# Kernel optimization log

Hardware: AMD Instinct MI355X
Metric: run time of the kernel (lower is better)

Reference implementation:

```python
import jax, jax.numpy as jnp
import numpy as np

N = 100000      # nodes
E = 3200000     # directed edges (avg degree 32)
F_IN = 128      # node feature dim
H = 16          # hidden_features
A = 10          # num_actions


def setup_inputs() -> dict:
    key = jax.random.key(0)
    ks = jax.random.split(key, 8)
    x = jax.random.normal(ks[0], (N, F_IN), dtype=jnp.float32)
    edge_index = jax.random.randint(ks[1], (2, E), 0, N, dtype=jnp.int32)
    W1 = jax.random.normal(ks[2], (F_IN, H), dtype=jnp.float32) * (1.0 / np.sqrt(F_IN))
    b1 = jnp.zeros((H,), dtype=jnp.float32)
    W2 = jax.random.normal(ks[3], (H, H), dtype=jnp.float32) * (1.0 / np.sqrt(H))
    b2 = jnp.zeros((H,), dtype=jnp.float32)
    Wc = jax.random.normal(ks[4], (H, A), dtype=jnp.float32) * (1.0 / np.sqrt(H))
    bc = jnp.zeros((A,), dtype=jnp.float32)
    return {"x": x, "edge_index": edge_index, "W1": W1, "b1": b1,
            "W2": W2, "b2": b2, "Wc": Wc, "bc": bc}


def _gcn_norm(edge_index, n_nodes):
    # PyG GCNConv: add self-loops, symmetric normalization deg^-1/2 A_hat deg^-1/2
    loop = jnp.arange(n_nodes, dtype=edge_index.dtype)
    src = jnp.concatenate([edge_index[0], loop])   # message sources
    dst = jnp.concatenate([edge_index[1], loop])   # aggregation targets
    deg = jax.ops.segment_sum(jnp.ones_like(dst, dtype=jnp.float32), dst,
                              num_segments=n_nodes)
    dis = jnp.where(deg > 0, jax.lax.rsqrt(deg), 0.0)  # deg^-1/2, inf -> 0
    norm = dis[src] * dis[dst]                          # [E + N]
    return src, dst, norm


def _gcn_conv(h, W, b, src, dst, norm, n_nodes):
    # transform first (small output dim), then gather/scale/scatter-add
    msg = (h @ W)[src] * norm[:, None]                  # [E+N, out]
    return jax.ops.segment_sum(msg, dst, num_segments=n_nodes) + b


def reference(x, edge_index, W1, b1, W2, b2, Wc, bc):
    n_nodes = x.shape[0]
    src, dst, norm = _gcn_norm(edge_index, n_nodes)
    h = jax.nn.relu(_gcn_conv(x, W1, b1, src, dst, norm, n_nodes))
    # F.dropout(training=False) is identity at inference
    h = jax.nn.relu(_gcn_conv(h, W2, b2, src, dst, norm, n_nodes))
    pooled = jnp.max(h, axis=0)                         # global MaxAggregation -> [H]
    return pooled @ Wc + bc                             # squeeze() -> [A]
```

## Files before the change

kernel.cpp:

```cpp
#include <hip/hip_runtime.h>
#include <hip/hip_fp16.h>


#define FIN 128
#define HDIM 16
#define AOUT 10
#define NPB 256
#define KMAX 512
#define TILE 4096
#define CAP 9216

typedef _Float16 f16x8 __attribute__((ext_vector_type(8)));
typedef float f32x4 __attribute__((ext_vector_type(4)));

__global__ void k_init(int* __restrict__ bcur, unsigned int* __restrict__ pooled,
                       int K) {
    int i = blockIdx.x * 256 + threadIdx.x;
    if (i < K) bcur[i] = i * CAP;
    if (i < 16) pooled[i] = 0u;
}

__global__ __launch_bounds__(256) void k_bin(const int* __restrict__ src,
                                             const int* __restrict__ dst, int E,
                                             int* __restrict__ bcur,
                                             unsigned int* __restrict__ pairs, int K) {
    __shared__ int hist[KMAX], lofs[KMAX], run[KMAX], gbase[KMAX], ss[256];
    __shared__ unsigned int buf[TILE];
    __shared__ unsigned short bkt[TILE];
    int t = threadIdx.x;
    int e0 = blockIdx.x * TILE;
    int e1 = min(E, e0 + TILE);
    for (int i = t; i < KMAX; i += 256) hist[i] = 0;
    __syncthreads();
    for (int e = e0 + t * 4; e < e1; e += 1024) {
        if (e + 4 <= e1) {
            int4 d4 = *reinterpret_cast<const int4*>(dst + e);
            atomicAdd(&hist[d4.x >> 8], 1);
            atomicAdd(&hist[d4.y >> 8], 1);
            atomicAdd(&hist[d4.z >> 8], 1);
            atomicAdd(&hist[d4.w >> 8], 1);
        } else {
            for (int q = e; q < e1; q++) atomicAdd(&hist[dst[q] >> 8], 1);
        }
    }
    __syncthreads();
    int a0 = hist[2 * t], a1 = hist[2 * t + 1];
    int psum = a0 + a1;
    ss[t] = psum;
    for (int d = 1; d < 256; d <<= 1) {
        __syncthreads();
        int add = (t >= d) ? ss[t - d] : 0;
        __syncthreads();
        ss[t] += add;
    }
    __syncthreads();
    int excl = ss[t] - psum;
    lofs[2 * t] = excl;          run[2 * t] = excl;
    lofs[2 * t + 1] = excl + a0; run[2 * t + 1] = excl + a0;
    __syncthreads();
    for (int b = t; b < K; b += 256)
        if (hist[b]) gbase[b] = atomicAdd(&bcur[b], hist[b]);
    __syncthreads();
    for (int e = e0 + t * 4; e < e1; e += 1024) {
        if (e + 4 <= e1) {
            int4 d4 = *reinterpret_cast<const int4*>(dst + e);
            int4 s4 = *reinterpret_cast<const int4*>(src + e);
            int b, r;
            b = d4.x >> 8; r = atomicAdd(&run[b], 1);
            buf[r] = (unsigned)s4.x | ((unsigned)(d4.x & 255) << 17); bkt[r] = (unsigned short)b;
            b = d4.y >> 8; r = atomicAdd(&run[b], 1);
            buf[r] = (unsigned)s4.y | ((unsigned)(d4.y & 255) << 17); bkt[r] = (unsigned short)b;
            b = d4.z >> 8; r = atomicAdd(&run[b], 1);
            buf[r] = (unsigned)s4.z | ((unsigned)(d4.z & 255) << 17); bkt[r] = (unsigned short)b;
            b = d4.w >> 8; r = atomicAdd(&run[b], 1);
            buf[r] = (unsigned)s4.w | ((unsigned)(d4.w & 255) << 17); bkt[r] = (unsigned short)b;
        } else {
            for (int q = e; q < e1; q++) {
                int d = dst[q], s = src[q], b = d >> 8;
                int r = atomicAdd(&run[b], 1);
                buf[r] = (unsigned)s | ((unsigned)(d & 255) << 17);
                bkt[r] = (unsigned short)b;
            }
        }
    }
    __syncthreads();
    int m = e1 - e0;
    for (int i = t; i < m; i += 256) {
        int b = bkt[i];
        pairs[gbase[b] + i - lofs[b]] = buf[i];
    }
}

__global__ __launch_bounds__(512) void k_sort(const unsigned int* __restrict__ pairs,
                                              const int* __restrict__ bcur,
                                              int* __restrict__ srcidx,
                                              int2* __restrict__ off2,
                                              float* __restrict__ dis, int n) {
    __shared__ int lcnt[NPB], pre[NPB], cur[NPB];
    int b = blockIdx.x, t = threadIdx.x;
    if (t < NPB) lcnt[t] = 0;
    __syncthreads();
    int base = b * CAP;
    int m = bcur[b] - base;
    for (int j = t; j < m; j += 512) atomicAdd(&lcnt[pairs[base + j] >> 17], 1);
    __syncthreads();
    int v = (t < NPB) ? lcnt[t] : 0;
    if (t < NPB) pre[t] = v;
    for (int d = 1; d < NPB; d <<= 1) {
        __syncthreads();
        int add = (t < NPB && t >= d) ? pre[t - d] : 0;
        __syncthreads();
        if (t < NPB) pre[t] += add;
    }
    __syncthreads();
    if (t < NPB) {
        int excl = pre[t] - v;
        cur[t] = excl;
        int node = (b << 8) + t;
        if (node < n) {
            off2[node] = make_int2(base + excl, base + excl + v);
            dis[node] = rsqrtf((float)(v + 1));
        }
    }
    __syncthreads();
    for (int j = t; j < m; j += 512) {
        unsigned p = pairs[base + j];
        int pos = base + atomicAdd(&cur[p >> 17], 1);
        srcidx[pos] = (int)(p & 0x1FFFF);
    }
}

__global__ __launch_bounds__(256) void k_gemm1(const float* __restrict__ x,
                                               const float* __restrict__ W1,
                                               const float* __restrict__ dis,
                                               __half* __restrict__ g16, int n) {
    int l = threadIdx.x & 63;
    int cc = l & 15, kg = l >> 4;
    f16x8 bfrag[4];
#pragma unroll
    for (int kc = 0; kc < 4; kc++)
#pragma unroll
        for (int j = 0; j < 8; j++)
            bfrag[kc][j] = (_Float16)W1[(kc * 32 + kg * 8 + j) * HDIM + cc];
    int tile = blockIdx.x * 4 + (threadIdx.x >> 6);
    int node0 = tile * 16;
    if (node0 >= n) return;
    const float* xr = x + (size_t)(node0 + cc) * FIN;
    f32x4 acc = {0.f, 0.f, 0.f, 0.f};
#pragma unroll
    for (int kc = 0; kc < 4; kc++) {
        float4 xa = *reinterpret_cast<const float4*>(xr + kc * 32 + kg * 8);
        float4 xb = *reinterpret_cast<const float4*>(xr + kc * 32 + kg * 8 + 4);
        f16x8 a;
        a[0] = (_Float16)xa.x; a[1] = (_Float16)xa.y;
        a[2] = (_Float16)xa.z; a[3] = (_Float16)xa.w;
        a[4] = (_Float16)xb.x; a[5] = (_Float16)xb.y;
        a[6] = (_Float16)xb.z; a[7] = (_Float16)xb.w;
        acc = __builtin_amdgcn_mfma_f32_16x16x32_f16(a, bfrag[kc], acc, 0, 0, 0);
    }
#pragma unroll
    for (int i = 0; i < 4; i++) {
        int nd = node0 + kg * 4 + i;
        g16[(size_t)nd * HDIM + cc] = (__half)(dis[nd] * acc[i]);
    }
}

__global__ __launch_bounds__(256) void k_gemm2(const float* __restrict__ h,
                                               const float* __restrict__ W2,
                                               const float* __restrict__ dis,
                                               __half* __restrict__ g16, int n) {
    int l = threadIdx.x & 63;
    int cc = l & 15, kg = l >> 4;
    f16x8 bfrag = {0, 0, 0, 0, 0, 0, 0, 0};
    if (kg < 2) {
#pragma unroll
        for (int j = 0; j < 8; j++)
            bfrag[j] = (_Float16)W2[(kg * 8 + j) * HDIM + cc];
    }
    int tile = blockIdx.x * 4 + (threadIdx.x >> 6);
    int node0 = tile * 16;
    if (node0 >= n) return;
    f16x8 a = {0, 0, 0, 0, 0, 0, 0, 0};
    if (kg < 2) {
        const float* hr = h + (size_t)(node0 + cc) * HDIM + kg * 8;
        float4 xa = *reinterpret_cast<const float4*>(hr);
        float4 xb = *reinterpret_cast<const float4*>(hr + 4);
        a[0] = (_Float16)xa.x; a[1] = (_Float16)xa.y;
        a[2] = (_Float16)xa.z; a[3] = (_Float16)xa.w;
        a[4] = (_Float16)xb.x; a[5] = (_Float16)xb.y;
        a[6] = (_Float16)xb.z; a[7] = (_Float16)xb.w;
    }
    f32x4 acc = {0.f, 0.f, 0.f, 0.f};
    acc = __builtin_amdgcn_mfma_f32_16x16x32_f16(a, bfrag, acc, 0, 0, 0);
#pragma unroll
    for (int i = 0; i < 4; i++) {
        int nd = node0 + kg * 4 + i;
        g16[(size_t)nd * HDIM + cc] = (__half)(dis[nd] * acc[i]);
    }
}

__global__ __launch_bounds__(256) void k_agg16(const __half* __restrict__ g16,
                                               const int2* __restrict__ off2,
                                               const int* __restrict__ srcidx,
                                               const float* __restrict__ dis,
                                               const float* __restrict__ bias,
                                               float* __restrict__ h, int n) {
    int tid = blockIdx.x * 256 + threadIdx.x;
    int node = tid >> 2, sub = tid & 3;
    int piece = sub & 1, half = sub >> 1;
    if (node >= n) return;
    const uint4* gp = reinterpret_cast<const uint4*>(g16);
    int2 oe = off2[node];
    int e0 = oe.x, e1 = oe.y;
    __half2 a0, a1, a2, a3;
    if (half == 0) {
        uint4 v = gp[(size_t)node * 2 + piece];
        a0 = __builtin_bit_cast(__half2, v.x);
        a1 = __builtin_bit_cast(__half2, v.y);
        a2 = __builtin_bit_cast(__half2, v.z);
        a3 = __builtin_bit_cast(__half2, v.w);
    } else {
        a0 = __half2{0, 0}; a1 = __half2{0, 0};
        a2 = __half2{0, 0}; a3 = __half2{0, 0};
    }
    int e = e0 + half;
    for (; e + 14 < e1; e += 16) {
        int s0 = srcidx[e];      int s1 = srcidx[e + 2];
        int s2 = srcidx[e + 4];  int s3 = srcidx[e + 6];
        int s4 = srcidx[e + 8];  int s5 = srcidx[e + 10];
        int s6 = srcidx[e + 12]; int s7 = srcidx[e + 14];
        uint4 w0 = gp[(size_t)s0 * 2 + piece];
        uint4 w1 = gp[(size_t)s1 * 2 + piece];
        uint4 w2 = gp[(size_t)s2 * 2 + piece];
        uint4 w3 = gp[(size_t)s3 * 2 + piece];
        uint4 w4 = gp[(size_t)s4 * 2 + piece];
        uint4 w5 = gp[(size_t)s5 * 2 + piece];
        uint4 w6 = gp[(size_t)s6 * 2 + piece];
        uint4 w7 = gp[(size_t)s7 * 2 + piece];
        a0 = __hadd2(a0, __builtin_bit_cast(__half2, w0.x));
        a1 = __hadd2(a1, __builtin_bit_cast(__half2, w0.y));
        a2 = __hadd2(a2, __builtin_bit_cast(__half2, w0.z));
        a3 = __hadd2(a3, __builtin_bit_cast(__half2, w0.w));
        a0 = __hadd2(a0, __builtin_bit_cast(__half2, w1.x));
        a1 = __hadd2(a1, __builtin_bit_cast(__half2, w1.y));
        a2 = __hadd2(a2, __builtin_bit_cast(__half2, w1.z));
        a3 = __hadd2(a3, __builtin_bit_cast(__half2, w1.w));
        a0 = __hadd2(a0, __builtin_bit_cast(__half2, w2.x));
        a1 = __hadd2(a1, __builtin_bit_cast(__half2, w2.y));
        a2 = __hadd2(a2, __builtin_bit_cast(__half2, w2.z));
        a3 = __hadd2(a3, __builtin_bit_cast(__half2, w2.w));
        a0 = __hadd2(a0, __builtin_bit_cast(__half2, w3.x));
        a1 = __hadd2(a1, __builtin_bit_cast(__half2, w3.y));
        a2 = __hadd2(a2, __builtin_bit_cast(__half2, w3.z));
        a3 = __hadd2(a3, __builtin_bit_cast(__half2, w3.w));
        a0 = __hadd2(a0, __builtin_bit_cast(__half2, w4.x));
        a1 = __hadd2(a1, __builtin_bit_cast(__half2, w4.y));
        a2 = __hadd2(a2, __builtin_bit_cast(__half2, w4.z));
        a3 = __hadd2(a3, __builtin_bit_cast(__half2, w4.w));
        a0 = __hadd2(a0, __builtin_bit_cast(__half2, w5.x));
        a1 = __hadd2(a1, __builtin_bit_cast(__half2, w5.y));
        a2 = __hadd2(a2, __builtin_bit_cast(__half2, w5.z));
        a3 = __hadd2(a3, __builtin_bit_cast(__half2, w5.w));
        a0 = __hadd2(a0, __builtin_bit_cast(__half2, w6.x));
        a1 = __hadd2(a1, __builtin_bit_cast(__half2, w6.y));
        a2 = __hadd2(a2, __builtin_bit_cast(__half2, w6.z));
        a3 = __hadd2(a3, __builtin_bit_cast(__half2, w6.w));
        a0 = __hadd2(a0, __builtin_bit_cast(__half2, w7.x));
        a1 = __hadd2(a1, __builtin_bit_cast(__half2, w7.y));
        a2 = __hadd2(a2, __builtin_bit_cast(__half2, w7.z));
        a3 = __hadd2(a3, __builtin_bit_cast(__half2, w7.w));
    }
    for (; e < e1; e += 2) {
        uint4 w = gp[(size_t)srcidx[e] * 2 + piece];
        a0 = __hadd2(a0, __builtin_bit_cast(__half2, w.x));
        a1 = __hadd2(a1, __builtin_bit_cast(__half2, w.y));
        a2 = __hadd2(a2, __builtin_bit_cast(__half2, w.z));
        a3 = __hadd2(a3, __builtin_bit_cast(__half2, w.w));
    }
    a0 = __hadd2(a0, __builtin_bit_cast(__half2, __shfl_xor(__builtin_bit_cast(unsigned, a0), 2)));
    a1 = __hadd2(a1, __builtin_bit_cast(__half2, __shfl_xor(__builtin_bit_cast(unsigned, a1), 2)));
    a2 = __hadd2(a2, __builtin_bit_cast(__half2, __shfl_xor(__builtin_bit_cast(unsigned, a2), 2)));
    a3 = __hadd2(a3, __builtin_bit_cast(__half2, __shfl_xor(__builtin_bit_cast(unsigned, a3), 2)));
    if (half == 0) {
        float dn = dis[node];
        const float* bp = bias + piece * 8;
        float2 f0 = __half22float2(a0), f1 = __half22float2(a1);
        float2 f2 = __half22float2(a2), f3 = __half22float2(a3);
        float4 o0, o1;
        o0.x = fmaxf(dn * f0.x + bp[0], 0.f); o0.y = fmaxf(dn * f0.y + bp[1], 0.f);
        o0.z = fmaxf(dn * f1.x + bp[2], 0.f); o0.w = fmaxf(dn * f1.y + bp[3], 0.f);
        o1.x = fmaxf(dn * f2.x + bp[4], 0.f); o1.y = fmaxf(dn * f2.y + bp[5], 0.f);
        o1.z = fmaxf(dn * f3.x + bp[6], 0.f); o1.w = fmaxf(dn * f3.y + bp[7], 0.f);
        float4* hp = reinterpret_cast<float4*>(h + (size_t)node * HDIM + piece * 8);
        hp[0] = o0; hp[1] = o1;
    }
}

__global__ __launch_bounds__(256) void k_maxpool(const float* __restrict__ h,
                                                 unsigned int* __restrict__ pooled, int n) {
    int t = threadIdx.x;
    int c = t & 15;
    int grp = t >> 4;
    float m = 0.f;
    for (int node = blockIdx.x * 16 + grp; node < n; node += gridDim.x * 16)
        m = fmaxf(m, h[(size_t)node * HDIM + c]);
    __shared__ float s[256];
    s[t] = m;
    __syncthreads();
    for (int d = 128; d >= 16; d >>= 1) {
        if (t < d) s[t] = fmaxf(s[t], s[t + d]);
        __syncthreads();
    }
    if (t < 16) atomicMax(&pooled[t], __float_as_uint(s[t]));
}

__global__ void k_final(const unsigned int* __restrict__ pooled, const float* __restrict__ Wc,
                        const float* __restrict__ bc, float* __restrict__ out) {
    __shared__ float p[HDIM];
    int t = threadIdx.x;
    if (t < HDIM) p[t] = __uint_as_float(pooled[t]);
    __syncthreads();
    if (t < AOUT) {
        float acc = bc[t];
#pragma unroll
        for (int c = 0; c < HDIM; c++) acc += p[c] * Wc[c * AOUT + t];
        out[t] = acc;
    }
}

extern "C" void kernel_launch(void* const* d_in, const int* in_sizes, int n_in,
                              void* d_out, int out_size, void* d_ws, size_t ws_size,
                              hipStream_t stream) {
    const float* x  = (const float*)d_in[0];
    const int*   ei = (const int*)d_in[1];
    const float* W1 = (const float*)d_in[2];
    const float* b1 = (const float*)d_in[3];
    const float* W2 = (const float*)d_in[4];
    const float* b2 = (const float*)d_in[5];
    const float* Wc = (const float*)d_in[6];
    const float* bc = (const float*)d_in[7];
    float* out = (float*)d_out;

    int n = in_sizes[0] / FIN;
    int E = in_sizes[1] / 2;
    const int* srcp = ei;
    const int* dstp = ei + E;
    int K = (n + NPB - 1) / NPB;

    char* ws = (char*)d_ws;
    auto alloc = [&](size_t bytes) -> char* {
        char* p = ws;
        ws += (bytes + 255) & ~(size_t)255;
        return p;
    };
    float*        dis   = (float*)alloc((size_t)n * 4);
    int*          bcur  = (int*)alloc((size_t)K * 4);
    int2*         off2  = (int2*)alloc((size_t)n * 8);
    unsigned int* pairs = (unsigned int*)alloc((size_t)K * CAP * 4);
    int*          srcidx= (int*)alloc((size_t)K * CAP * 4);
    __half*       g16   = (__half*)alloc((size_t)n * HDIM * 2);
    float*        h     = (float*)alloc((size_t)n * HDIM * 4);
    unsigned int* pooled= (unsigned int*)alloc(64);

    k_init<<<(K + 255) / 256, 256, 0, stream>>>(bcur, pooled, K);
    k_bin<<<(E + TILE - 1) / TILE, 256, 0, stream>>>(srcp, dstp, E, bcur, pairs, K);
    k_sort<<<K, 512, 0, stream>>>(pairs, bcur, srcidx, off2, dis, n);

    int ntile = (n + 15) / 16;
    int gblocks = (ntile + 3) / 4;
    k_gemm1<<<gblocks, 256, 0, stream>>>(x, W1, dis, g16, n);
    k_agg16<<<(4 * n + 255) / 256, 256, 0, stream>>>(g16, off2, srcidx, dis, b1, h, n);
    k_gemm2<<<gblocks, 256, 0, stream>>>(h, W2, dis, g16, n);
    k_agg16<<<(4 * n + 255) / 256, 256, 0, stream>>>(g16, off2, srcidx, dis, b2, h, n);

    k_maxpool<<<256, 256, 0, stream>>>(h, pooled, n);
    k_final<<<1, 64, 0, stream>>>(pooled, Wc, bc, out);
}
```

Before: 145.4 us.

## Pad CSR rows to multiples of four and fuse max-pool into second aggregation

k_sort now pads each node's edge segment to a multiple of 4, filling the padding with a dummy source index n that points at a zeroed extra row of g16. This lets the aggregation kernel load source indices as int4 vectors instead of strided scalar loads. The second aggregation is templated to fold max-pooling in with shuffle and shared-memory reductions plus atomicMax, which drops the h write, the separate maxpool kernel and its re-read of h. In exchange the sort kernel writes extra padding entries, CAP grows to absorb the padding, and the gather reads extra dummy rows.

Measured after the change: 137.7 us. -5.3%, faster.

```diff
diff --git a/kernel.cpp b/kernel.cpp
--- a/kernel.cpp
+++ b/kernel.cpp
@@ -8,16 +8,17 @@
 #define NPB 256
 #define KMAX 512
 #define TILE 4096
-#define CAP 9216
+#define CAP 10240
 
 typedef _Float16 f16x8 __attribute__((ext_vector_type(8)));
 typedef float f32x4 __attribute__((ext_vector_type(4)));
 
 __global__ void k_init(int* __restrict__ bcur, unsigned int* __restrict__ pooled,
-                       int K) {
+                       unsigned int* __restrict__ gz, int K) {
     int i = blockIdx.x * 256 + threadIdx.x;
     if (i < K) bcur[i] = i * CAP;
     if (i < 16) pooled[i] = 0u;
+    if (i < 8) gz[i] = 0u;
 }
 
 __global__ __launch_bounds__(256) void k_bin(const int* __restrict__ src,
@@ -105,7 +106,8 @@
     for (int j = t; j < m; j += 512) atomicAdd(&lcnt[pairs[base + j] >> 17], 1);
     __syncthreads();
     int v = (t < NPB) ? lcnt[t] : 0;
-    if (t < NPB) pre[t] = v;
+    int w = (v + 3) & ~3;
+    if (t < NPB) pre[t] = w;
     for (int d = 1; d < NPB; d <<= 1) {
         __syncthreads();
         int add = (t < NPB && t >= d) ? pre[t - d] : 0;
@@ -114,13 +116,14 @@
     }
     __syncthreads();
     if (t < NPB) {
-        int excl = pre[t] - v;
-        cur[t] = excl;
+        int start = pre[t] - w;
+        cur[t] = start;
         int node = (b << 8) + t;
         if (node < n) {
-            off2[node] = make_int2(base + excl, base + excl + v);
+            off2[node] = make_int2(base + start, base + start + v);
             dis[node] = rsqrtf((float)(v + 1));
         }
+        for (int p = v; p < w; p++) srcidx[base + start + p] = n;
     }
     __syncthreads();
     for (int j = t; j < m; j += 512) {
@@ -199,119 +202,99 @@
     }
 }
 
+#define ACC4(V) \
+    a0 = __hadd2(a0, __builtin_bit_cast(__half2, (V).x)); \
+    a1 = __hadd2(a1, __builtin_bit_cast(__half2, (V).y)); \
+    a2 = __hadd2(a2, __builtin_bit_cast(__half2, (V).z)); \
+    a3 = __hadd2(a3, __builtin_bit_cast(__half2, (V).w));
+
+template <int POOL>
 __global__ __launch_bounds__(256) void k_agg16(const __half* __restrict__ g16,
                                                const int2* __restrict__ off2,
                                                const int* __restrict__ srcidx,
                                                const float* __restrict__ dis,
                                                const float* __restrict__ bias,
-                                               float* __restrict__ h, int n) {
-    int tid = blockIdx.x * 256 + threadIdx.x;
-    int node = tid >> 2, sub = tid & 3;
+                                               float* __restrict__ h,
+                                               unsigned int* __restrict__ pooled,
+                                               int n) {
+    __shared__ float smax[4][16];
+    int t = threadIdx.x;
+    int tid = blockIdx.x * 256 + t;
+    int node = tid >> 2, sub = t & 3;
     int piece = sub & 1, half = sub >> 1;
-    if (node >= n) return;
-    const uint4* gp = reinterpret_cast<const uint4*>(g16);
-    int2 oe = off2[node];
-    int e0 = oe.x, e1 = oe.y;
-    __half2 a0, a1, a2, a3;
-    if (half == 0) {
-        uint4 v = gp[(size_t)node * 2 + piece];
-        a0 = __builtin_bit_cast(__half2, v.x);
-        a1 = __builtin_bit_cast(__half2, v.y);
-        a2 = __builtin_bit_cast(__half2, v.z);
-        a3 = __builtin_bit_cast(__half2, v.w);
-    } else {
-        a0 = __half2{0, 0}; a1 = __half2{0, 0};
-        a2 = __half2{0, 0}; a3 = __half2{0, 0};
-    }
-    int e = e0 + half;
-    for (; e + 14 < e1; e += 16) {
-        int s0 = srcidx[e];      int s1 = srcidx[e + 2];
-        int s2 = srcidx[e + 4];  int s3 = srcidx[e + 6];
-        int s4 = srcidx[e + 8];  int s5 = srcidx[e + 10];
-        int s6 = srcidx[e + 12]; int s7 = srcidx[e + 14];
-        uint4 w0 = gp[(size_t)s0 * 2 + piece];
-        uint4 w1 = gp[(size_t)s1 * 2 + piece];
-        uint4 w2 = gp[(size_t)s2 * 2 + piece];
-        uint4 w3 = gp[(size_t)s3 * 2 + piece];
-        uint4 w4 = gp[(size_t)s4 * 2 + piece];
-        uint4 w5 = gp[(size_t)s5 * 2 + piece];
-        uint4 w6 = gp[(size_t)s6 * 2 + piece];
-        uint4 w7 = gp[(size_t)s7 * 2 + piece];
-        a0 = __hadd2(a0, __builtin_bit_cast(__half2, w0.x));
-        a1 = __hadd2(a1, __builtin_bit_cast(__half2, w0.y));
-        a2 = __hadd2(a2, __builtin_bit_cast(__half2, w0.z));
-        a3 = __hadd2(a3, __builtin_bit_cast(__half2, w0.w));
-        a0 = __hadd2(a0, __builtin_bit_cast(__half2, w1.x));
-        a1 = __hadd2(a1, __builtin_bit_cast(__half2, w1.y));
-        a2 = __hadd2(a2, __builtin_bit_cast(__half2, w1.z));
-        a3 = __hadd2(a3, __builtin_bit_cast(__half2, w1.w));
-        a0 = __hadd2(a0, __builtin_bit_cast(__half2, w2.x));
-        a1 = __hadd2(a1, __builtin_bit_cast(__half2, w2.y));
-        a2 = __hadd2(a2, __builtin_bit_cast(__half2, w2.z));
-        a3 = __hadd2(a3, __builtin_bit_cast(__half2, w2.w));
-        a0 = __hadd2(a0, __builtin_bit_cast(__half2, w3.x));
-        a1 = __hadd2(a1, __builtin_bit_cast(__half2, w3.y));
-        a2 = __hadd2(a2, __builtin_bit_cast(__half2, w3.z));
-        a3 = __hadd2(a3, __builtin_bit_cast(__half2, w3.w));
-        a0 = __hadd2(a0, __builtin_bit_cast(__half2, w4.x));
-        a1 = __hadd2(a1, __builtin_bit_cast(__half2, w4.y));
-        a2 = __hadd2(a2, __builtin_bit_cast(__half2, w4.z));
-        a3 = __hadd2(a3, __builtin_bit_cast(__half2, w4.w));
-        a0 = __hadd2(a0, __builtin_bit_cast(__half2, w5.x));
-        a1 = __hadd2(a1, __builtin_bit_cast(__half2, w5.y));
-        a2 = __hadd2(a2, __builtin_bit_cast(__half2, w5.z));
-        a3 = __hadd2(a3, __builtin_bit_cast(__half2, w5.w));
-        a0 = __hadd2(a0, __builtin_bit_cast(__half2, w6.x));
-        a1 = __hadd2(a1, __builtin_bit_cast(__half2, w6.y));
-        a2 = __hadd2(a2, __builtin_bit_cast(__half2, w6.z));
-        a3 = __hadd2(a3, __builtin_bit_cast(__half2, w6.w));
-        a0 = __hadd2(a0, __builtin_bit_cast(__half2, w7.x));
-        a1 = __hadd2(a1, __builtin_bit_cast(__half2, w7.y));
-        a2 = __hadd2(a2, __builtin_bit_cast(__half2, w7.z));
-        a3 = __hadd2(a3, __builtin_bit_cast(__half2, w7.w));
-    }
-    for (; e < e1; e += 2) {
-        uint4 w = gp[(size_t)srcidx[e] * 2 + piece];
-        a0 = __hadd2(a0, __builtin_bit_cast(__half2, w.x));
-        a1 = __hadd2(a1, __builtin_bit_cast(__half2, w.y));
-        a2 = __hadd2(a2, __builtin_bit_cast(__half2, w.z));
-        a3 = __hadd2(a3, __builtin_bit_cast(__half2, w.w));
-    }
-    a0 = __hadd2(a0, __builtin_bit_cast(__half2, __shfl_xor(__builtin_bit_cast(unsigned, a0), 2)));
-    a1 = __hadd2(a1, __builtin_bit_cast(__half2, __shfl_xor(__builtin_bit_cast(unsigned, a1), 2)));
-    a2 = __hadd2(a2, __builtin_bit_cast(__half2, __shfl_xor(__builtin_bit_cast(unsigned, a2), 2)));
-    a3 = __hadd2(a3, __builtin_bit_cast(__half2, __shfl_xor(__builtin_bit_cast(unsigned, a3), 2)));
-    if (half == 0) {
-        float dn = dis[node];
-        const float* bp = bias + piece * 8;
-        float2 f0 = __half22float2(a0), f1 = __half22float2(a1);
-        float2 f2 = __half22float2(a2), f3 = __half22float2(a3);
-        float4 o0, o1;
-        o0.x = fmaxf(dn * f0.x + bp[0], 0.f); o0.y = fmaxf(dn * f0.y + bp[1], 0.f);
-        o0.z = fmaxf(dn * f1.x + bp[2], 0.f); o0.w = fmaxf(dn * f1.y + bp[3], 0.f);
-        o1.x = fmaxf(dn * f2.x + bp[4], 0.f); o1.y = fmaxf(dn * f2.y + bp[5], 0.f);
-        o1.z = fmaxf(dn * f3.x + bp[6], 0.f); o1.w = fmaxf(dn * f3.y + bp[7], 0.f);
-        float4* hp = reinterpret_cast<float4*>(h + (size_t)node * HDIM + piece * 8);
-        hp[0] = o0; hp[1] = o1;
-    }
-}
-
-__global__ __launch_bounds__(256) void k_maxpool(const float* __restrict__ h,
-                                                 unsigned int* __restrict__ pooled, int n) {
-    int t = threadIdx.x;
-    int c = t & 15;
-    int grp = t >> 4;
-    float m = 0.f;
-    for (int node = blockIdx.x * 16 + grp; node < n; node += gridDim.x * 16)
-        m = fmaxf(m, h[(size_t)node * HDIM + c]);
-    __shared__ float s[256];
-    s[t] = m;
-    __syncthreads();
-    for (int d = 128; d >= 16; d >>= 1) {
-        if (t < d) s[t] = fmaxf(s[t], s[t + d]);
-        __syncthreads();
-    }
-    if (t < 16) atomicMax(&pooled[t], __float_as_uint(s[t]));
+    bool active = node < n;
+    float4 o0 = {0.f, 0.f, 0.f, 0.f}, o1 = {0.f, 0.f, 0.f, 0.f};
+    if (active) {
+        const uint4* gp = reinterpret_cast<const uint4*>(g16);
+        int2 oe = off2[node];
+        int e0 = oe.x, e1 = oe.y;
+        __half2 a0{0, 0}, a1{0, 0}, a2{0, 0}, a3{0, 0};
+        if (half == 0) {
+            uint4 v = gp[(size_t)node * 2 + piece];
+            ACC4(v)
+        }
+        int e = e0 + 4 * half;
+        for (; e + 8 < e1; e += 16) {
+            int4 sa = *reinterpret_cast<const int4*>(srcidx + e);
+            int4 sb = *reinterpret_cast<const int4*>(srcidx + e + 8);
+            uint4 w0 = gp[(size_t)sa.x * 2 + piece];
+            uint4 w1 = gp[(size_t)sa.y * 2 + piece];
+            uint4 w2 = gp[(size_t)sa.z * 2 + piece];
+            uint4 w3 = gp[(size_t)sa.w * 2 + piece];
+            uint4 w4 = gp[(size_t)sb.x * 2 + piece];
+            uint4 w5 = gp[(size_t)sb.y * 2 + piece];
+            uint4 w6 = gp[(size_t)sb.z * 2 + piece];
+            uint4 w7 = gp[(size_t)sb.w * 2 + piece];
+            ACC4(w0) ACC4(w1) ACC4(w2) ACC4(w3)
+            ACC4(w4) ACC4(w5) ACC4(w6) ACC4(w7)
+        }
+        for (; e < e1; e += 8) {
+            int4 sa = *reinterpret_cast<const int4*>(srcidx + e);
+            uint4 w0 = gp[(size_t)sa.x * 2 + piece];
+            uint4 w1 = gp[(size_t)sa.y * 2 + piece];
+            uint4 w2 = gp[(size_t)sa.z * 2 + piece];
+            uint4 w3 = gp[(size_t)sa.w * 2 + piece];
+            ACC4(w0) ACC4(w1) ACC4(w2) ACC4(w3)
+        }
+        a0 = __hadd2(a0, __builtin_bit_cast(__half2, __shfl_xor(__builtin_bit_cast(unsigned, a0), 2)));
+        a1 = __hadd2(a1, __builtin_bit_cast(__half2, __shfl_xor(__builtin_bit_cast(unsigned, a1), 2)));
+        a2 = __hadd2(a2, __builtin_bit_cast(__half2, __shfl_xor(__builtin_bit_cast(unsigned, a2), 2)));
+        a3 = __hadd2(a3, __builtin_bit_cast(__half2, __shfl_xor(__builtin_bit_cast(unsigned, a3), 2)));
+        if (half == 0) {
+            float dn = dis[node];
+            const float* bp = bias + piece * 8;
+            float2 f0 = __half22float2(a0), f1 = __half22float2(a1);
+            float2 f2 = __half22float2(a2), f3 = __half22float2(a3);
+            o0.x = fmaxf(dn * f0.x + bp[0], 0.f); o0.y = fmaxf(dn * f0.y + bp[1], 0.f);
+            o0.z = fmaxf(dn * f1.x + bp[2], 0.f); o0.w = fmaxf(dn * f1.y + bp[3], 0.f);
+            o1.x = fmaxf(dn * f2.x + bp[4], 0.f); o1.y = fmaxf(dn * f2.y + bp[5], 0.f);
+            o1.z = fmaxf(dn * f3.x + bp[6], 0.f); o1.w = fmaxf(dn * f3.y + bp[7], 0.f);
+            if (!POOL) {
+                float4* hp = reinterpret_cast<float4*>(h + (size_t)node * HDIM + piece * 8);
+                hp[0] = o0; hp[1] = o1;
+            }
+        }
+    }
+    if (POOL) {
+#pragma unroll
+        for (int d = 4; d <= 32; d <<= 1) {
+            o0.x = fmaxf(o0.x, __shfl_xor(o0.x, d)); o0.y = fmaxf(o0.y, __shfl_xor(o0.y, d));
+            o0.z = fmaxf(o0.z, __shfl_xor(o0.z, d)); o0.w = fmaxf(o0.w, __shfl_xor(o0.w, d));
+            o1.x = fmaxf(o1.x, __shfl_xor(o1.x, d)); o1.y = fmaxf(o1.y, __shfl_xor(o1.y, d));
+            o1.z = fmaxf(o1.z, __shfl_xor(o1.z, d)); o1.w = fmaxf(o1.w, __shfl_xor(o1.w, d));
+        }
+        int wv = t >> 6;
+        if ((t & 63) < 2) {
+            float* sp = &smax[wv][piece * 8];
+            sp[0] = o0.x; sp[1] = o0.y; sp[2] = o0.z; sp[3] = o0.w;
+            sp[4] = o1.x; sp[5] = o1.y; sp[6] = o1.z; sp[7] = o1.w;
+        }
+        __syncthreads();
+        if (t < 16) {
+            float m = fmaxf(fmaxf(smax[0][t], smax[1][t]), fmaxf(smax[2][t], smax[3][t]));
+            atomicMax(&pooled[t], __float_as_uint(m));
+        }
+    }
 }
 
 __global__ void k_final(const unsigned int* __restrict__ pooled, const float* __restrict__ Wc,
@@ -358,21 +341,23 @@
     int2*         off2  = (int2*)alloc((size_t)n * 8);
     unsigned int* pairs = (unsigned int*)alloc((size_t)K * CAP * 4);
     int*          srcidx= (int*)alloc((size_t)K * CAP * 4);
-    __half*       g16   = (__half*)alloc((size_t)n * HDIM * 2);
+    __half*       g16   = (__half*)alloc((size_t)(n + 1) * HDIM * 2);
     float*        h     = (float*)alloc((size_t)n * HDIM * 4);
     unsigned int* pooled= (unsigned int*)alloc(64);
 
-    k_init<<<(K + 255) / 256, 256, 0, stream>>>(bcur, pooled, K);
+    k_init<<<(K + 255) / 256, 256, 0, stream>>>(bcur, pooled,
+                                                (unsigned int*)(g16 + (size_t)n * HDIM), K);
     k_bin<<<(E + TILE - 1) / TILE, 256, 0, stream>>>(srcp, dstp, E, bcur, pairs, K);
     k_sort<<<K, 512, 0, stream>>>(pairs, bcur, srcidx, off2, dis, n);
 
     int ntile = (n + 15) / 16;
     int gblocks = (ntile + 3) / 4;
     k_gemm1<<<gblocks, 256, 0, stream>>>(x, W1, dis, g16, n);
-    k_agg16<<<(4 * n + 255) / 256, 256, 0, stream>>>(g16, off2, srcidx, dis, b1, h, n);
+    k_agg16<0><<<(4 * n + 255) / 256, 256, 0, stream>>>(g16, off2, srcidx, dis, b1,
+                                                        h, pooled, n);
     k_gemm2<<<gblocks, 256, 0, stream>>>(h, W2, dis, g16, n);
-    k_agg16<<<(4 * n + 255) / 256, 256, 0, stream>>>(g16, off2, srcidx, dis, b2, h, n);
-
-    k_maxpool<<<256, 256, 0, stream>>>(h, pooled, n);
+    k_agg16<1><<<(4 * n + 255) / 256, 256, 0, stream>>>(g16, off2, srcidx, dis, b2,
+                                                        nullptr, pooled, n);
+
     k_final<<<1, 64, 0, stream>>>(pooled, Wc, bc, out);
 }
```
